# Optimization experiments

Measured on AMD Instinct MI355X. Metric: run time of the kernel, lower is better.

## Reference

```python
import jax, jax.numpy as jnp
import numpy as np

N = 100000        # nodes
E = 1600000       # edges (avg degree 16)
D = 128           # feature dim (in_dim == out_dim)
L = 3             # num_layers
P = 8             # num_parts


def setup_inputs() -> dict:
    key = jax.random.key(0)
    k1, k2, k3, k4, k5, k6 = jax.random.split(key, 6)
    edge_row = jnp.sort(jax.random.randint(k1, (E,), 0, N))
    edge_col = jax.random.randint(k2, (E,), 0, N)
    edge_vals = jax.random.uniform(k3, (E,), dtype=jnp.float32)
    x = jax.random.normal(k4, (N, D), dtype=jnp.float32)
    stacked_params = jax.random.normal(k5, (L, D, D, P), dtype=jnp.float32)
    layer_weights = jax.random.normal(k6, (L, P), dtype=jnp.float32)
    return {"edge_row": edge_row, "edge_col": edge_col, "edge_vals": edge_vals,
            "x": x, "stacked_params": stacked_params, "layer_weights": layer_weights}


def reference(edge_row, edge_col, edge_vals, x, stacked_params, layer_weights):
    n = x.shape[0]
    num_layers = stacked_params.shape[0]
    h = x
    for i in range(num_layers):
        # sparse adj.spmm(h): gather source features, scale by edge value, sum per row
        msg = h[edge_col] * edge_vals[:, None]                       # [E, D]
        ax = jax.ops.segment_sum(msg, edge_row, num_segments=n)      # [N, D]
        # MyLinear: softmax over the num_parts weight, contract parts dim
        w = jax.nn.softmax(layer_weights[i])                         # [P]
        ww = jnp.einsum('oip,p->oi', stacked_params[i], w)           # [D_out, D_in]
        h = ax @ ww.T                                                # [N, D_out]
        if i < num_layers - 1:
            h = jax.nn.relu(h)
    return h
```

## Files before the change

kernel.cpp:

```cpp
#include <hip/hip_runtime.h>
#include <cstdint>

#define D 128
#define P 8
#define L 3

typedef __attribute__((ext_vector_type(8))) _Float16 f16x8;
typedef __attribute__((ext_vector_type(4))) float    f32x4;
typedef __attribute__((ext_vector_type(2))) float    f32x2;

#if __has_builtin(__builtin_amdgcn_cvt_pk_f32_fp8) && __has_builtin(__builtin_amdgcn_cvt_pk_fp8_f32)
#define HAVE_FP8_CVT 1
#else
#define HAVE_FP8_CVT 0
#endif

template<bool HI>
static __device__ __forceinline__ f32x2 fp8_pair(uint32_t u) {
#if HAVE_FP8_CVT
    return __builtin_amdgcn_cvt_pk_f32_fp8((int)u, HI);
#else
    uint32_t w = HI ? (u >> 16) : u;
    f32x2 r;
#pragma unroll
    for (int i = 0; i < 2; i++) {
        uint32_t b = (w >> (8 * i)) & 0xffu;
        uint32_t mag = b & 0x7fu;
        uint16_t h = (uint16_t)(((b & 0x80u) << 8) | ((mag >= 8u) ? ((mag << 7) + 0x2000u) : 0u));
        union { uint16_t q; _Float16 hf; } c; c.q = h;
        r[i] = (float)c.hf;
    }
    return r;
#endif
}

static __device__ __forceinline__ uint32_t f32_to_fp8(float v) {
#if HAVE_FP8_CVT
    return (uint32_t)__builtin_amdgcn_cvt_pk_fp8_f32(v, v, 0, false) & 0xffu;
#else
    union { _Float16 hf; uint16_t q; } c; c.hf = (_Float16)v;
    uint32_t s = ((uint32_t)c.q >> 8) & 0x80u;
    int t = (int)(c.q & 0x7fff) - 0x2000;
    if (t < 0) return s;
    int r = (t + 63 + ((t >> 7) & 1)) >> 7;
    if (r > 0x7e) r = 0x7e;
    return s | (uint32_t)r;
#endif
}

__global__ void prep_edges(const int* __restrict__ er, const int* __restrict__ col,
                           const float* __restrict__ vals,
                           int* __restrict__ rp, uint32_t* __restrict__ epk,
                           int n, int e) {
    int i = blockIdx.x * blockDim.x + threadIdx.x;
    if (i >= e) return;
    union { _Float16 h; uint16_t u; } v;
    v.h = (_Float16)vals[i];
    epk[i] = ((uint32_t)col[i] << 15) | (uint32_t)(v.u & 0x7FFFu);

    int cur = er[i];
    if (i == 0) {
        for (int r = 0; r <= cur; r++) rp[r] = 0;
    } else {
        int prev = er[i - 1];
        for (int r = prev + 1; r <= cur; r++) rp[r] = i;
    }
    if (i == e - 1) {
        for (int r = cur + 1; r <= n; r++) rp[r] = e;
    }
}

__global__ void build_ww(const float* __restrict__ sp, const float* __restrict__ lw,
                         _Float16* __restrict__ wwB) {
    int idx = blockIdx.x * blockDim.x + threadIdx.x;
    if (idx >= L * D * D) return;
    int l = idx / (D * D);
    int rem = idx - l * D * D;
    int o = rem / D;
    int i = rem - o * D;
    float wv[P];
    float m = -1e30f;
#pragma unroll
    for (int p = 0; p < P; p++) { wv[p] = lw[l * P + p]; m = fmaxf(m, wv[p]); }
    float s = 0.f;
#pragma unroll
    for (int p = 0; p < P; p++) { wv[p] = __expf(wv[p] - m); s += wv[p]; }
    float inv = 1.0f / s;
    const float* spp = sp + ((size_t)(l * D + o) * D + i) * P;
    float acc = 0.f;
#pragma unroll
    for (int p = 0; p < P; p++) acc += spp[p] * wv[p];
    int kt = i >> 5, kp = i & 31;
    wwB[(((l * 4 + kt) * D + o) << 5) + kp] = (_Float16)(acc * inv);
}

static __device__ __forceinline__ void mfma_store16_q8(const _Float16 (*s_h)[136],
                                                       const _Float16* __restrict__ wwB_l,
                                                       uint8_t* __restrict__ y8,
                                                       float* __restrict__ scl,
                                                       unsigned* srow,
                                                       int row0, int n, int tid) {
    const int w = tid >> 6, lane = tid & 63;
    const int quad = lane >> 4, l16 = lane & 15;
    f32x4 acc[2] = {};
#pragma unroll
    for (int kt = 0; kt < 4; kt++) {
        f16x8 af = *(const f16x8*)&s_h[l16][kt * 32 + quad * 8];
#pragma unroll
        for (int c = 0; c < 2; c++) {
            const int ct = w * 2 + c;
            f16x8 bf = *(const f16x8*)&wwB_l[((kt * D + ct * 16 + l16) << 5) + quad * 8];
            acc[c] = __builtin_amdgcn_mfma_f32_16x16x32_f16(af, bf, acc[c], 0, 0, 0);
        }
    }
#pragma unroll
    for (int rg = 0; rg < 4; rg++) {
        float m = fmaxf(fabsf(acc[0][rg]), fabsf(acc[1][rg]));
#pragma unroll
        for (int d = 1; d < 16; d <<= 1) m = fmaxf(m, __shfl_xor(m, d));
        if (l16 == 0) atomicMax(&srow[quad * 4 + rg], __float_as_uint(m));
    }
    __syncthreads();
#pragma unroll
    for (int rg = 0; rg < 4; rg++) {
        const int rr = quad * 4 + rg;
        const int row = row0 + rr;
        float rmax = fmaxf(__uint_as_float(srow[rr]), 1e-20f);
        float qs = 448.f / rmax;
        if (row < n) {
#pragma unroll
            for (int c = 0; c < 2; c++) {
                const int ct = w * 2 + c;
                float v = acc[c][rg] * qs;
                v = fminf(fmaxf(v, -448.f), 448.f);
                y8[row * D + ct * 16 + l16] = (uint8_t)f32_to_fp8(v);
            }
            if (w == 0 && l16 == 0) scl[row] = rmax * (1.f / 448.f);
        }
    }
}

__global__ __launch_bounds__(256, 8)
void gemm_x32(const float* __restrict__ x, const _Float16* __restrict__ wwB_l,
              uint8_t* __restrict__ y8, float* __restrict__ scl, int n) {
    __shared__ _Float16 s_h[16][136];
    __shared__ unsigned srow[16];
    const int tid = threadIdx.x;
    const int row0 = blockIdx.x * 16;
    const int c8 = (tid & 15) * 8;
    if (tid < 16) srow[tid] = 0;
    {
        int r = tid >> 4;
        int row = row0 + r;
        float4 v0 = {}, v1 = {};
        if (row < n) {
            v0 = *(const float4*)&x[row * D + c8];
            v1 = *(const float4*)&x[row * D + c8 + 4];
        }
        f16x8 h;
        h[0] = (_Float16)v0.x; h[1] = (_Float16)v0.y;
        h[2] = (_Float16)v0.z; h[3] = (_Float16)v0.w;
        h[4] = (_Float16)v1.x; h[5] = (_Float16)v1.y;
        h[6] = (_Float16)v1.z; h[7] = (_Float16)v1.w;
        *(f16x8*)&s_h[r][c8] = h;
    }
    __syncthreads();
    mfma_store16_q8(s_h, wwB_l, y8, scl, srow, row0, n, tid);
}

template<int NB>
static __device__ __forceinline__ void gather_chunk8(float (&a)[8],
                                                     const uint8_t* __restrict__ y8,
                                                     const uint32_t* __restrict__ epk,
                                                     const float* __restrict__ scl,
                                                     int e, int c8) {
    uint32_t m[NB];
#pragma unroll
    for (int j = 0; j < NB; j++) m[j] = epk[e + j];
    uint2 g[NB]; float sc[NB];
#pragma unroll
    for (int j = 0; j < NB; j++) {
        uint32_t row = m[j] >> 15;
        g[j]  = *(const uint2*)&y8[row * (uint32_t)D + (uint32_t)c8];
        sc[j] = scl[row];
    }
#pragma unroll
    for (int j = 0; j < NB; j++) {
        union { uint16_t u; _Float16 h; } vv; vv.u = (uint16_t)(m[j] & 0x7FFFu);
        float vf = (float)vv.h * sc[j];
        f32x2 p;
        p = fp8_pair<false>(g[j].x); a[0] += vf * p[0]; a[1] += vf * p[1];
        p = fp8_pair<true >(g[j].x); a[2] += vf * p[0]; a[3] += vf * p[1];
        p = fp8_pair<false>(g[j].y); a[4] += vf * p[0]; a[5] += vf * p[1];
        p = fp8_pair<true >(g[j].y); a[6] += vf * p[0]; a[7] += vf * p[1];
    }
}

static __device__ __forceinline__ void gather_row8(float (&a)[8],
                                                   const uint8_t* __restrict__ y8,
                                                   const uint32_t* __restrict__ epk,
                                                   const float* __restrict__ scl,
                                                   int e, int e1, int c8) {
    for (; e + 8 <= e1; e += 8) gather_chunk8<8>(a, y8, epk, scl, e, c8);
    if (e + 4 <= e1) { gather_chunk8<4>(a, y8, epk, scl, e, c8); e += 4; }
    for (; e < e1; e++) gather_chunk8<1>(a, y8, epk, scl, e, c8);
}

__global__ __launch_bounds__(256, 6)
void fused_layer(const uint8_t* __restrict__ yprev, const float* __restrict__ sprev,
                 const int* __restrict__ rp, const uint32_t* __restrict__ epk,
                 const _Float16* __restrict__ wwB_l,
                 uint8_t* __restrict__ ynext, float* __restrict__ snext, int n) {
    __shared__ _Float16 s_h[16][136];
    __shared__ unsigned srow[16];
    const int tid = threadIdx.x;
    const int row0 = blockIdx.x * 16;
    const int sg = tid >> 4;
    const int c8 = (tid & 15) * 8;
    if (tid < 16) srow[tid] = 0;
    {
        int r = row0 + sg;
        float a[8] = {0.f, 0.f, 0.f, 0.f, 0.f, 0.f, 0.f, 0.f};
        if (r < n) gather_row8(a, yprev, epk, sprev, rp[r], rp[r + 1], c8);
        f16x8 o;
#pragma unroll
        for (int k = 0; k < 8; k++) o[k] = (_Float16)fmaxf(a[k], 0.f);
        *(f16x8*)&s_h[sg][c8] = o;
    }
    __syncthreads();
    mfma_store16_q8(s_h, wwB_l, ynext, snext, srow, row0, n, tid);
}

__global__ __launch_bounds__(256, 6)
void spmm_f32(const uint8_t* __restrict__ y8, const float* __restrict__ sprev,
              const int* __restrict__ rp, const uint32_t* __restrict__ epk,
              float* __restrict__ out, int n) {
    const int tid = threadIdx.x;
    const int r = blockIdx.x * 16 + (tid >> 4);
    const int c8 = (tid & 15) * 8;
    if (r >= n) return;
    float a[8] = {0.f, 0.f, 0.f, 0.f, 0.f, 0.f, 0.f, 0.f};
    gather_row8(a, y8, epk, sprev, rp[r], rp[r + 1], c8);
    *(float4*)&out[(size_t)r * D + c8]     = make_float4(a[0], a[1], a[2], a[3]);
    *(float4*)&out[(size_t)r * D + c8 + 4] = make_float4(a[4], a[5], a[6], a[7]);
}

extern "C" void kernel_launch(void* const* d_in, const int* in_sizes, int n_in,
                              void* d_out, int out_size, void* d_ws, size_t ws_size,
                              hipStream_t stream) {
    const int*   edge_row  = (const int*)d_in[0];
    const int*   edge_col  = (const int*)d_in[1];
    const float* edge_vals = (const float*)d_in[2];
    const float* x         = (const float*)d_in[3];
    const float* sp        = (const float*)d_in[4];
    const float* lw        = (const float*)d_in[5];
    float* out = (float*)d_out;

    const int E_ = in_sizes[0];
    const int N_ = in_sizes[3] / D;

    char* ws = (char*)d_ws;
    int* row_ptr = (int*)ws;
    size_t off = (((size_t)(N_ + 1) * sizeof(int)) + 255) & ~(size_t)255;
    uint32_t* epk = (uint32_t*)(ws + off);
    off += (size_t)E_ * sizeof(uint32_t);
    off = (off + 255) & ~(size_t)255;
    _Float16* wwB = (_Float16*)(ws + off);
    off += (size_t)L * 4 * D * 32 * sizeof(_Float16);
    off = (off + 255) & ~(size_t)255;
    uint8_t* y8A = (uint8_t*)(ws + off);
    off += (size_t)N_ * D;
    uint8_t* y8B = (uint8_t*)(ws + off);
    off += (size_t)N_ * D;
    off = (off + 255) & ~(size_t)255;
    float* scA = (float*)(ws + off);
    off += (size_t)N_ * sizeof(float);
    float* scB = (float*)(ws + off);

    prep_edges<<<(E_ + 255) / 256, 256, 0, stream>>>(edge_row, edge_col, edge_vals,
                                                     row_ptr, epk, N_, E_);
    build_ww<<<(L * D * D + 255) / 256, 256, 0, stream>>>(sp, lw, wwB);

    const int sblk = (N_ + 15) / 16;
    const int WWL = 4 * D * 32;

    gemm_x32<<<sblk, 256, 0, stream>>>(x, wwB, y8A, scA, N_);
    fused_layer<<<sblk, 256, 0, stream>>>(y8A, scA, row_ptr, epk, wwB + WWL,     y8B, scB, N_);
    fused_layer<<<sblk, 256, 0, stream>>>(y8B, scB, row_ptr, epk, wwB + 2 * WWL, y8A, scA, N_);
    spmm_f32<<<sblk, 256, 0, stream>>>(y8A, scA, row_ptr, epk, out, N_);
}
```

Measured before the change: 266.7 us.

## Process 32 rows per block with 16-byte fp8 gathers per lane

Each block now covers 32 rows instead of 16. The MFMA epilogue computes two 16-row tiles, so every B-fragment load from the weight matrix feeds two MFMAs. In the SpMM gathers each lane reads 16 fp8 columns (uint4) instead of 8, so 8 lanes cover a row, which halves the number of gather instructions and edge-metadata loads per row. A sched_barrier keeps the loads grouped ahead of the math. The cost is more registers per thread (16 accumulators, 4 accumulator tiles), occupancy lowered to 5 waves, and fewer lanes working on each row, which hurts latency hiding on low-degree rows.

Result: slower. 636.4 us (+138.6%).

```diff
diff --git a/kernel.cpp b/kernel.cpp
--- a/kernel.cpp
+++ b/kernel.cpp
@@ -94,7 +94,7 @@
     wwB[(((l * 4 + kt) * D + o) << 5) + kp] = (_Float16)(acc * inv);
 }
 
-static __device__ __forceinline__ void mfma_store16_q8(const _Float16 (*s_h)[136],
+static __device__ __forceinline__ void mfma_store32_q8(const _Float16 (*s_h)[136],
                                                        const _Float16* __restrict__ wwB_l,
                                                        uint8_t* __restrict__ y8,
                                                        float* __restrict__ scl,
@@ -102,40 +102,48 @@
                                                        int row0, int n, int tid) {
     const int w = tid >> 6, lane = tid & 63;
     const int quad = lane >> 4, l16 = lane & 15;
-    f32x4 acc[2] = {};
+    f32x4 acc[2][2] = {};
 #pragma unroll
     for (int kt = 0; kt < 4; kt++) {
-        f16x8 af = *(const f16x8*)&s_h[l16][kt * 32 + quad * 8];
+        f16x8 af0 = *(const f16x8*)&s_h[l16][kt * 32 + quad * 8];
+        f16x8 af1 = *(const f16x8*)&s_h[16 + l16][kt * 32 + quad * 8];
 #pragma unroll
         for (int c = 0; c < 2; c++) {
             const int ct = w * 2 + c;
             f16x8 bf = *(const f16x8*)&wwB_l[((kt * D + ct * 16 + l16) << 5) + quad * 8];
-            acc[c] = __builtin_amdgcn_mfma_f32_16x16x32_f16(af, bf, acc[c], 0, 0, 0);
-        }
-    }
-#pragma unroll
-    for (int rg = 0; rg < 4; rg++) {
-        float m = fmaxf(fabsf(acc[0][rg]), fabsf(acc[1][rg]));
-#pragma unroll
-        for (int d = 1; d < 16; d <<= 1) m = fmaxf(m, __shfl_xor(m, d));
-        if (l16 == 0) atomicMax(&srow[quad * 4 + rg], __float_as_uint(m));
+            acc[0][c] = __builtin_amdgcn_mfma_f32_16x16x32_f16(af0, bf, acc[0][c], 0, 0, 0);
+            acc[1][c] = __builtin_amdgcn_mfma_f32_16x16x32_f16(af1, bf, acc[1][c], 0, 0, 0);
+        }
+    }
+#pragma unroll
+    for (int rt = 0; rt < 2; rt++) {
+#pragma unroll
+        for (int rg = 0; rg < 4; rg++) {
+            float m = fmaxf(fabsf(acc[rt][0][rg]), fabsf(acc[rt][1][rg]));
+#pragma unroll
+            for (int d = 1; d < 16; d <<= 1) m = fmaxf(m, __shfl_xor(m, d));
+            if (l16 == 0) atomicMax(&srow[rt * 16 + quad * 4 + rg], __float_as_uint(m));
+        }
     }
     __syncthreads();
 #pragma unroll
-    for (int rg = 0; rg < 4; rg++) {
-        const int rr = quad * 4 + rg;
-        const int row = row0 + rr;
-        float rmax = fmaxf(__uint_as_float(srow[rr]), 1e-20f);
-        float qs = 448.f / rmax;
-        if (row < n) {
-#pragma unroll
-            for (int c = 0; c < 2; c++) {
-                const int ct = w * 2 + c;
-                float v = acc[c][rg] * qs;
-                v = fminf(fmaxf(v, -448.f), 448.f);
-                y8[row * D + ct * 16 + l16] = (uint8_t)f32_to_fp8(v);
+    for (int rt = 0; rt < 2; rt++) {
+#pragma unroll
+        for (int rg = 0; rg < 4; rg++) {
+            const int rr = rt * 16 + quad * 4 + rg;
+            const int row = row0 + rr;
+            float rmax = fmaxf(__uint_as_float(srow[rr]), 1e-20f);
+            float qs = 448.f / rmax;
+            if (row < n) {
+#pragma unroll
+                for (int c = 0; c < 2; c++) {
+                    const int ct = w * 2 + c;
+                    float v = acc[rt][c][rg] * qs;
+                    v = fminf(fmaxf(v, -448.f), 448.f);
+                    y8[row * D + ct * 16 + l16] = (uint8_t)f32_to_fp8(v);
+                }
+                if (w == 0 && l16 == 0) scl[row] = rmax * (1.f / 448.f);
             }
-            if (w == 0 && l16 == 0) scl[row] = rmax * (1.f / 448.f);
         }
     }
 }
@@ -143,106 +151,122 @@
 __global__ __launch_bounds__(256, 8)
 void gemm_x32(const float* __restrict__ x, const _Float16* __restrict__ wwB_l,
               uint8_t* __restrict__ y8, float* __restrict__ scl, int n) {
-    __shared__ _Float16 s_h[16][136];
-    __shared__ unsigned srow[16];
+    __shared__ _Float16 s_h[32][136];
+    __shared__ unsigned srow[32];
     const int tid = threadIdx.x;
-    const int row0 = blockIdx.x * 16;
+    const int row0 = blockIdx.x * 32;
     const int c8 = (tid & 15) * 8;
-    if (tid < 16) srow[tid] = 0;
+    if (tid < 32) srow[tid] = 0;
     {
         int r = tid >> 4;
-        int row = row0 + r;
-        float4 v0 = {}, v1 = {};
-        if (row < n) {
-            v0 = *(const float4*)&x[row * D + c8];
-            v1 = *(const float4*)&x[row * D + c8 + 4];
-        }
-        f16x8 h;
-        h[0] = (_Float16)v0.x; h[1] = (_Float16)v0.y;
-        h[2] = (_Float16)v0.z; h[3] = (_Float16)v0.w;
-        h[4] = (_Float16)v1.x; h[5] = (_Float16)v1.y;
-        h[6] = (_Float16)v1.z; h[7] = (_Float16)v1.w;
-        *(f16x8*)&s_h[r][c8] = h;
+#pragma unroll
+        for (int h2 = 0; h2 < 2; h2++) {
+            int rr = r + h2 * 16;
+            int row = row0 + rr;
+            float4 v0 = {}, v1 = {};
+            if (row < n) {
+                v0 = *(const float4*)&x[row * D + c8];
+                v1 = *(const float4*)&x[row * D + c8 + 4];
+            }
+            f16x8 h;
+            h[0] = (_Float16)v0.x; h[1] = (_Float16)v0.y;
+            h[2] = (_Float16)v0.z; h[3] = (_Float16)v0.w;
+            h[4] = (_Float16)v1.x; h[5] = (_Float16)v1.y;
+            h[6] = (_Float16)v1.z; h[7] = (_Float16)v1.w;
+            *(f16x8*)&s_h[rr][c8] = h;
+        }
     }
     __syncthreads();
-    mfma_store16_q8(s_h, wwB_l, y8, scl, srow, row0, n, tid);
+    mfma_store32_q8(s_h, wwB_l, y8, scl, srow, row0, n, tid);
 }
 
 template<int NB>
-static __device__ __forceinline__ void gather_chunk8(float (&a)[8],
-                                                     const uint8_t* __restrict__ y8,
-                                                     const uint32_t* __restrict__ epk,
-                                                     const float* __restrict__ scl,
-                                                     int e, int c8) {
+static __device__ __forceinline__ void gather_chunk16(float (&a)[16],
+                                                      const uint8_t* __restrict__ y8,
+                                                      const uint32_t* __restrict__ epk,
+                                                      const float* __restrict__ scl,
+                                                      int e, int c16) {
     uint32_t m[NB];
 #pragma unroll
     for (int j = 0; j < NB; j++) m[j] = epk[e + j];
-    uint2 g[NB]; float sc[NB];
+    uint4 g[NB]; float sc[NB];
 #pragma unroll
     for (int j = 0; j < NB; j++) {
         uint32_t row = m[j] >> 15;
-        g[j]  = *(const uint2*)&y8[row * (uint32_t)D + (uint32_t)c8];
+        g[j]  = *(const uint4*)&y8[row * (uint32_t)D + (uint32_t)c16];
         sc[j] = scl[row];
     }
+    __builtin_amdgcn_sched_barrier(0);
 #pragma unroll
     for (int j = 0; j < NB; j++) {
         union { uint16_t u; _Float16 h; } vv; vv.u = (uint16_t)(m[j] & 0x7FFFu);
         float vf = (float)vv.h * sc[j];
         f32x2 p;
-        p = fp8_pair<false>(g[j].x); a[0] += vf * p[0]; a[1] += vf * p[1];
-        p = fp8_pair<true >(g[j].x); a[2] += vf * p[0]; a[3] += vf * p[1];
-        p = fp8_pair<false>(g[j].y); a[4] += vf * p[0]; a[5] += vf * p[1];
-        p = fp8_pair<true >(g[j].y); a[6] += vf * p[0]; a[7] += vf * p[1];
-    }
-}
-
-static __device__ __forceinline__ void gather_row8(float (&a)[8],
-                                                   const uint8_t* __restrict__ y8,
-                                                   const uint32_t* __restrict__ epk,
-                                                   const float* __restrict__ scl,
-                                                   int e, int e1, int c8) {
-    for (; e + 8 <= e1; e += 8) gather_chunk8<8>(a, y8, epk, scl, e, c8);
-    if (e + 4 <= e1) { gather_chunk8<4>(a, y8, epk, scl, e, c8); e += 4; }
-    for (; e < e1; e++) gather_chunk8<1>(a, y8, epk, scl, e, c8);
-}
-
-__global__ __launch_bounds__(256, 6)
+        p = fp8_pair<false>(g[j].x); a[ 0] += vf * p[0]; a[ 1] += vf * p[1];
+        p = fp8_pair<true >(g[j].x); a[ 2] += vf * p[0]; a[ 3] += vf * p[1];
+        p = fp8_pair<false>(g[j].y); a[ 4] += vf * p[0]; a[ 5] += vf * p[1];
+        p = fp8_pair<true >(g[j].y); a[ 6] += vf * p[0]; a[ 7] += vf * p[1];
+        p = fp8_pair<false>(g[j].z); a[ 8] += vf * p[0]; a[ 9] += vf * p[1];
+        p = fp8_pair<true >(g[j].z); a[10] += vf * p[0]; a[11] += vf * p[1];
+        p = fp8_pair<false>(g[j].w); a[12] += vf * p[0]; a[13] += vf * p[1];
+        p = fp8_pair<true >(g[j].w); a[14] += vf * p[0]; a[15] += vf * p[1];
+    }
+}
+
+static __device__ __forceinline__ void gather_row16(float (&a)[16],
+                                                    const uint8_t* __restrict__ y8,
+                                                    const uint32_t* __restrict__ epk,
+                                                    const float* __restrict__ scl,
+                                                    int e, int e1, int c16) {
+    for (; e + 8 <= e1; e += 8) gather_chunk16<8>(a, y8, epk, scl, e, c16);
+    if (e + 4 <= e1) { gather_chunk16<4>(a, y8, epk, scl, e, c16); e += 4; }
+    for (; e < e1; e++) gather_chunk16<1>(a, y8, epk, scl, e, c16);
+}
+
+__global__ __launch_bounds__(256, 5)
 void fused_layer(const uint8_t* __restrict__ yprev, const float* __restrict__ sprev,
                  const int* __restrict__ rp, const uint32_t* __restrict__ epk,
                  const _Float16* __restrict__ wwB_l,
                  uint8_t* __restrict__ ynext, float* __restrict__ snext, int n) {
-    __shared__ _Float16 s_h[16][136];
-    __shared__ unsigned srow[16];
+    __shared__ _Float16 s_h[32][136];
+    __shared__ unsigned srow[32];
     const int tid = threadIdx.x;
-    const int row0 = blockIdx.x * 16;
-    const int sg = tid >> 4;
-    const int c8 = (tid & 15) * 8;
-    if (tid < 16) srow[tid] = 0;
+    const int row0 = blockIdx.x * 32;
+    const int sg = tid >> 3;
+    const int c16 = (tid & 7) * 16;
+    if (tid < 32) srow[tid] = 0;
     {
         int r = row0 + sg;
-        float a[8] = {0.f, 0.f, 0.f, 0.f, 0.f, 0.f, 0.f, 0.f};
-        if (r < n) gather_row8(a, yprev, epk, sprev, rp[r], rp[r + 1], c8);
-        f16x8 o;
-#pragma unroll
-        for (int k = 0; k < 8; k++) o[k] = (_Float16)fmaxf(a[k], 0.f);
-        *(f16x8*)&s_h[sg][c8] = o;
+        float a[16] = {};
+        if (r < n) gather_row16(a, yprev, epk, sprev, rp[r], rp[r + 1], c16);
+        f16x8 o0, o1;
+#pragma unroll
+        for (int k = 0; k < 8; k++) {
+            o0[k] = (_Float16)fmaxf(a[k], 0.f);
+            o1[k] = (_Float16)fmaxf(a[8 + k], 0.f);
+        }
+        *(f16x8*)&s_h[sg][c16]     = o0;
+        *(f16x8*)&s_h[sg][c16 + 8] = o1;
     }
     __syncthreads();
-    mfma_store16_q8(s_h, wwB_l, ynext, snext, srow, row0, n, tid);
-}
-
-__global__ __launch_bounds__(256, 6)
+    mfma_store32_q8(s_h, wwB_l, ynext, snext, srow, row0, n, tid);
+}
+
+__global__ __launch_bounds__(256, 5)
 void spmm_f32(const uint8_t* __restrict__ y8, const float* __restrict__ sprev,
               const int* __restrict__ rp, const uint32_t* __restrict__ epk,
               float* __restrict__ out, int n) {
     const int tid = threadIdx.x;
-    const int r = blockIdx.x * 16 + (tid >> 4);
-    const int c8 = (tid & 15) * 8;
+    const int r = blockIdx.x * 32 + (tid >> 3);
+    const int c16 = (tid & 7) * 16;
     if (r >= n) return;
-    float a[8] = {0.f, 0.f, 0.f, 0.f, 0.f, 0.f, 0.f, 0.f};
-    gather_row8(a, y8, epk, sprev, rp[r], rp[r + 1], c8);
-    *(float4*)&out[(size_t)r * D + c8]     = make_float4(a[0], a[1], a[2], a[3]);
-    *(float4*)&out[(size_t)r * D + c8 + 4] = make_float4(a[4], a[5], a[6], a[7]);
+    float a[16] = {};
+    gather_row16(a, y8, epk, sprev, rp[r], rp[r + 1], c16);
+    float* o = &out[(size_t)r * D + c16];
+    *(float4*)&o[ 0] = make_float4(a[ 0], a[ 1], a[ 2], a[ 3]);
+    *(float4*)&o[ 4] = make_float4(a[ 4], a[ 5], a[ 6], a[ 7]);
+    *(float4*)&o[ 8] = make_float4(a[ 8], a[ 9], a[10], a[11]);
+    *(float4*)&o[12] = make_float4(a[12], a[13], a[14], a[15]);
 }
 
 extern "C" void kernel_launch(void* const* d_in, const int* in_sizes, int n_in,
@@ -281,7 +305,7 @@
                                                      row_ptr, epk, N_, E_);
     build_ww<<<(L * D * D + 255) / 256, 256, 0, stream>>>(sp, lw, wwB);
 
-    const int sblk = (N_ + 15) / 16;
+    const int sblk = (N_ + 31) / 32;
     const int WWL = 4 * D * 32;
 
     gemm_x32<<<sblk, 256, 0, stream>>>(x, wwB, y8A, scA, N_);
```
